# Kernel optimization log

Hardware: AMD Instinct MI355X
Metric: run time of the kernel (lower is better)

## Reference

```python
import jax, jax.numpy as jnp
import numpy as np

H = 512
N = 512
BSZ = 8
L = 4096
DIRECTION = 2  # 0=forward, 1=backward, 2=bidirectional (split N in half)


def setup_inputs() -> dict:
    key = jax.random.key(0)
    k = jax.random.split(key, 6)
    u = jax.random.normal(k[0], (BSZ, L, H), jnp.float32)
    # variable lengths in [L//2, L]
    lengths = jax.random.randint(k[1], (BSZ,), L // 2, L + 1).astype(jnp.int32)
    # LRU init: r_min=0, r_max=1, max_phase=2*pi
    u1 = jax.random.uniform(k[2], (N,), jnp.float32)
    nu_log = jnp.log(-0.5 * jnp.log(u1))
    u2 = jax.random.uniform(k[3], (N,), jnp.float32)
    theta_log = jnp.log(2.0 * np.pi * u2)
    lam = jnp.exp(-jnp.exp(nu_log) + 1j * jnp.exp(theta_log))  # (N,) complex
    gamma = jnp.sqrt(1.0 - jnp.abs(lam) ** 2)[:, None]          # (N,1)
    B = jax.random.normal(k[4], (H, N, 2), jnp.float32) / np.float32(np.sqrt(2 * H)) * gamma
    C = jax.random.normal(k[5], (2, H, N), jnp.float32) / np.float32(np.sqrt(N))
    return {"u": u, "lengths": lengths, "nu_log": nu_log, "theta_log": theta_log, "B": B, "C": C}


def _lru_scan(lam, Bu, reverse):
    """Diagonal linear recurrence x_t = lam * x_{t-1} + Bu_t along axis 2 via associative scan.
    lam: (n,) complex; Bu: (B, n, L) complex."""
    a = jnp.broadcast_to(lam[None, :, None], Bu.shape)

    def op(e1, e2):
        a1, b1 = e1
        a2, b2 = e2
        return a1 * a2, a2 * b1 + b2

    _, x = jax.lax.associative_scan(op, (a, Bu), axis=2, reverse=reverse)
    return x


def reference(u, lengths, nu_log, theta_log, B, C):
    lam = jnp.exp(-jnp.exp(nu_log) + 1j * jnp.exp(theta_log))  # (N,)
    Bc = B[..., 0] + 1j * B[..., 1]                            # (H, N) complex
    Bu = jnp.einsum('blh,hn->bnl', u, Bc)                      # (B, N, L) complex
    mask = jnp.arange(L)[None, :] < lengths[:, None]           # (B, L)
    Bu = Bu * mask[:, None, :]
    if DIRECTION == 2:
        h = N // 2
        x = jnp.concatenate([
            _lru_scan(lam[:h], Bu[:, :h], reverse=False),
            _lru_scan(lam[h:], Bu[:, h:], reverse=True),
        ], axis=1)
    elif DIRECTION == 0:
        x = _lru_scan(lam, Bu, reverse=False)
    else:
        x = _lru_scan(lam, Bu, reverse=True)
    x = x * mask[:, None, :]           # zero outputs past each sequence length
    x = jnp.swapaxes(x, 1, 2)          # (B, L, N)
    y = x.real @ C[0] - x.imag @ C[1]  # (B, L, H)  (requires H == N, as in source)
    return y
```

## Files before the change

kernel.cpp:

```cpp
#include <hip/hip_runtime.h>

#define L_SEQ   4096
#define BSZQ    8
#define ROWS    (BSZQ * L_SEQ)
#define KC1     512
#define NC1     1024
#define KC2     1024
#define NC2     512
#define CHUNK   64
#define NCHUNK  64

typedef __attribute__((ext_vector_type(8))) short bfrag;
typedef __attribute__((ext_vector_type(4))) float ffrag;

static __device__ __forceinline__ unsigned short f2bf(float f) {
    union { float f; unsigned int u; } v; v.f = f;
    unsigned int r = v.u + 0x7fffu + ((v.u >> 16) & 1u);
    return (unsigned short)(r >> 16);
}
static __device__ __forceinline__ unsigned int pk2(float a, float b) {
    return (unsigned int)f2bf(a) | ((unsigned int)f2bf(b) << 16);
}
static __device__ __forceinline__ float2 unpk2(unsigned int u) {
    union { unsigned int u; float f; } a, b;
    a.u = u << 16;
    b.u = u & 0xffff0000u;
    return make_float2(a.f, b.f);
}

static __device__ __forceinline__ void async16(const void* g, void* l) {
    __builtin_amdgcn_global_load_lds(
        (const __attribute__((address_space(1))) unsigned int*)g,
        (__attribute__((address_space(3))) unsigned int*)l,
        16, 0, 0);
}

__global__ __launch_bounds__(256) void prep_all_kernel(
    const float* __restrict__ B, const float* __restrict__ C,
    const float* __restrict__ nu_log, const float* __restrict__ theta_log,
    unsigned short* __restrict__ Bt, unsigned short* __restrict__ Dt,
    float2* __restrict__ lam)
{
    int g = blockIdx.x, tid = threadIdx.x;
    if (g < 2048) {
        int idx = g * 256 + tid;
        int n2 = idx >> 9, h = idx & 511;
        Bt[idx] = f2bf(B[(size_t)h * 1024 + n2]);
    } else if (g < 4096) {
        int idx = (g - 2048) * 256 + tid;
        int j = idx >> 10, k = idx & 1023;
        int n = k >> 1, c = k & 1;
        float v = C[((size_t)c * 512 + n) * 512 + j];
        Dt[idx] = f2bf(c ? -v : v);
    } else {
#pragma unroll
        for (int r = 0; r < 2; r++) {
            int n = tid + r * 256;
            float mag = expf(-expf(nu_log[n]));
            float th  = expf(theta_log[n]);
            lam[n] = make_float2(mag * cosf(th), mag * sinf(th));
        }
    }
}

__global__ __launch_bounds__(256) void conv_mask_kernel(
    const float* __restrict__ u, const int* __restrict__ lengths,
    unsigned short* __restrict__ ub)
{
    int idx = blockIdx.x * 256 + threadIdx.x;
    int row = idx >> 6;
    int l = row & (L_SEQ - 1), b = row >> 12;
    bool keep = (l < lengths[b]);
    union { unsigned int s[4]; float4 f; } o;
    if (keep) {
        const float4 a = *(const float4*)(u + (size_t)idx * 8);
        const float4 c = *(const float4*)(u + (size_t)idx * 8 + 4);
        o.s[0] = pk2(a.x, a.y); o.s[1] = pk2(a.z, a.w);
        o.s[2] = pk2(c.x, c.y); o.s[3] = pk2(c.z, c.w);
    } else {
        o.s[0] = o.s[1] = o.s[2] = o.s[3] = 0u;
    }
    *(float4*)(ub + (size_t)idx * 8) = o.f;
}

template<int KD, int ND, bool BF16OUT>
__global__ __launch_bounds__(256, 4) void gemm_db(
    const unsigned short* __restrict__ A,
    const unsigned short* __restrict__ Bt,
    void* __restrict__ Co)
{
    __shared__ __align__(16) unsigned short As[2][128 * 32];
    __shared__ __align__(16) unsigned short Bs[2][128 * 32];

    const int tid  = threadIdx.x;
    const int lane = tid & 63, w = tid >> 6;
    const int q = lane >> 4, m16 = lane & 15;
    const int wr = (w >> 1) * 64, wc = (w & 1) * 64;
    const int row0 = blockIdx.x * 128;
    const int col0 = blockIdx.y * 128;

    ffrag acc[4][4];
#pragma unroll
    for (int i = 0; i < 4; i++)
#pragma unroll
        for (int j = 0; j < 4; j++) acc[i][j] = (ffrag)0.f;

#define STAGE_T(GP, TB, KT, GR0) do {                                          \
    _Pragma("unroll")                                                          \
    for (int j_ = 0; j_ < 2; j_++) {                                           \
        int s_ = j_ * 256 + tid;                                               \
        int r_ = s_ >> 2;                                                      \
        int cs_ = (s_ & 3) ^ ((r_ >> 1) & 3);                                  \
        async16(GP + (size_t)((GR0) + r_) * KD + (KT) + cs_ * 8,               \
                &TB[(size_t)(j_ * 256 + w * 64) * 8]);                         \
    }                                                                          \
} while (0)

    STAGE_T(A,  As[0], 0, row0);
    STAGE_T(Bt, Bs[0], 0, col0);
    __syncthreads();

    int c = 0;
    for (int kt = 0; kt < KD; kt += 32) {
        if (kt + 32 < KD) {
            STAGE_T(A,  As[c ^ 1], kt + 32, row0);
            STAGE_T(Bt, Bs[c ^ 1], kt + 32, col0);
        }
        bfrag a[4], b[4];
#pragma unroll
        for (int ri = 0; ri < 4; ri++) {
            int r_ = wr + ri * 16 + m16;
            a[ri] = *(const bfrag*)&As[c][r_ * 32 + (q ^ ((r_ >> 1) & 3)) * 8];
        }
#pragma unroll
        for (int ci = 0; ci < 4; ci++) {
            int r_ = wc + ci * 16 + m16;
            b[ci] = *(const bfrag*)&Bs[c][r_ * 32 + (q ^ ((r_ >> 1) & 3)) * 8];
        }
#pragma unroll
        for (int ri = 0; ri < 4; ri++)
#pragma unroll
            for (int ci = 0; ci < 4; ci++)
                acc[ri][ci] = __builtin_amdgcn_mfma_f32_16x16x32_bf16(
                    a[ri], b[ci], acc[ri][ci], 0, 0, 0);
        __syncthreads();
        c ^= 1;
    }
#undef STAGE_T

    if (BF16OUT) {
        unsigned int* Cb = (unsigned int*)Co;
        const int colc0 = (col0 >> 1) + (w & 1) * 32;
#pragma unroll
        for (int ri = 0; ri < 4; ri++)
#pragma unroll
            for (int cp = 0; cp < 2; cp++)
#pragma unroll
                for (int r4 = 0; r4 < 4; r4++) {
                    float a0 = acc[ri][cp * 2][r4];
                    float a1 = acc[ri][cp * 2 + 1][r4];
                    float b0 = __shfl_xor(a0, 1);
                    float b1 = __shfl_xor(a1, 1);
                    unsigned int uo = (m16 & 1) ? pk2(b1, a1) : pk2(a0, b0);
                    int row = row0 + wr + ri * 16 + q * 4 + r4;
                    int ccol = (cp * 2 + (m16 & 1)) * 8 + (m16 >> 1);
                    Cb[(size_t)row * (ND / 2) + colc0 + ccol] = uo;
                }
    } else {
        float* Cf = (float*)Co;
#pragma unroll
        for (int ri = 0; ri < 4; ri++)
#pragma unroll
            for (int r4 = 0; r4 < 4; r4++) {
                int row = row0 + wr + ri * 16 + q * 4 + r4;
#pragma unroll
                for (int ci = 0; ci < 4; ci++) {
                    int col = col0 + wc + ci * 16 + m16;
                    Cf[(size_t)row * ND + col] = acc[ri][ci][r4];
                }
            }
    }
}

__global__ __launch_bounds__(256) void scan_states_kernel(
    const unsigned int* __restrict__ bu, const float2* __restrict__ lam,
    float2* __restrict__ states)
{
    int t = threadIdx.x;
    int b = blockIdx.x >> 6;
    int c = blockIdx.x & 63;
    float4 lm = *(const float4*)&lam[2 * t];
    float x0r = 0.f, x0i = 0.f, x1r = 0.f, x1i = 0.f;
    bool fwd = (t < 128);
    int l0 = fwd ? (c * CHUNK) : (c * CHUNK + CHUNK - 1);
    const unsigned int* p = bu + ((size_t)b * L_SEQ + l0) * 512 + 2 * t;
    ptrdiff_t step = fwd ? 512 : -512;
#pragma unroll 8
    for (int i = 0; i < CHUNK; i++) {
        uint2 v = *(const uint2*)p;
        float2 v0 = unpk2(v.x), v1 = unpk2(v.y);
        float n0r = lm.x * x0r - lm.y * x0i + v0.x;
        float n0i = lm.x * x0i + lm.y * x0r + v0.y;
        float n1r = lm.z * x1r - lm.w * x1i + v1.x;
        float n1i = lm.z * x1i + lm.w * x1r + v1.y;
        x0r = n0r; x0i = n0i; x1r = n1r; x1i = n1i;
        p += step;
    }
    *(float4*)&states[((size_t)b * NCHUNK + c) * 512 + 2 * t] =
        make_float4(x0r, x0i, x1r, x1i);
}

__global__ __launch_bounds__(256) void scan_fix_apply_kernel(
    unsigned int* __restrict__ bu, const float2* __restrict__ states,
    const float2* __restrict__ lam, const int* __restrict__ lengths)
{
    int t = threadIdx.x;
    int b = blockIdx.x >> 6;
    int c = blockIdx.x & 63;
    int len = lengths[b];
    bool fwd = (t < 128);
    float4 lm = *(const float4*)&lam[2 * t];

    float a0r = lm.x, a0i = lm.y, a1r = lm.z, a1i = lm.w;
#pragma unroll
    for (int i = 0; i < 6; i++) {
        float n0r = a0r * a0r - a0i * a0i; a0i = 2.f * a0r * a0i; a0r = n0r;
        float n1r = a1r * a1r - a1i * a1i; a1i = 2.f * a1r * a1i; a1r = n1r;
    }

    float c0r = 0.f, c0i = 0.f, c1r = 0.f, c1i = 0.f;
    for (int g = 0; g < 8; ++g) {
        float4 s[8];
#pragma unroll
        for (int k = 0; k < 8; ++k) {
            int cc = fwd ? (g * 8 + k) : (63 - (g * 8 + k));
            s[k] = *(const float4*)&states[((size_t)b * NCHUNK + cc) * 512 + 2 * t];
        }
#pragma unroll
        for (int k = 0; k < 8; ++k) {
            int cc = fwd ? (g * 8 + k) : (63 - (g * 8 + k));
            bool use = fwd ? (cc < c) : (cc > c);
            if (use) {
                float n0r = a0r * c0r - a0i * c0i + s[k].x;
                float n0i = a0r * c0i + a0i * c0r + s[k].y;
                float n1r = a1r * c1r - a1i * c1i + s[k].z;
                float n1i = a1r * c1i + a1i * c1r + s[k].w;
                c0r = n0r; c0i = n0i; c1r = n1r; c1i = n1i;
            }
        }
    }

    int l0 = fwd ? (c * CHUNK) : (c * CHUNK + CHUNK - 1);
    int dl = fwd ? 1 : -1;
    unsigned int* p = bu + ((size_t)b * L_SEQ + l0) * 512 + 2 * t;
    ptrdiff_t step = fwd ? 512 : -512;
    float x0r = c0r, x0i = c0i, x1r = c1r, x1i = c1i;
    int l = l0;
#pragma unroll 8
    for (int i = 0; i < CHUNK; i++) {
        uint2 v = *(const uint2*)p;
        float2 v0 = unpk2(v.x), v1 = unpk2(v.y);
        float n0r = lm.x * x0r - lm.y * x0i + v0.x;
        float n0i = lm.x * x0i + lm.y * x0r + v0.y;
        float n1r = lm.z * x1r - lm.w * x1i + v1.x;
        float n1i = lm.z * x1i + lm.w * x1r + v1.y;
        x0r = n0r; x0i = n0i; x1r = n1r; x1i = n1i;
        uint2 o2;
        o2.x = (l >= len) ? 0u : pk2(x0r, x0i);
        o2.y = (l >= len) ? 0u : pk2(x1r, x1i);
        *(uint2*)p = o2;
        p += step; l += dl;
    }
}

extern "C" void kernel_launch(void* const* d_in, const int* in_sizes, int n_in,
                              void* d_out, int out_size, void* d_ws, size_t ws_size,
                              hipStream_t stream)
{
    const float* u        = (const float*)d_in[0];
    const int*   lengths  = (const int*)  d_in[1];
    const float* nu_log   = (const float*)d_in[2];
    const float* theta_log= (const float*)d_in[3];
    const float* B        = (const float*)d_in[4];
    const float* C        = (const float*)d_in[5];
    float* y = (float*)d_out;

    char* wp = (char*)d_ws;
    float2* lam     = (float2*)wp;  wp += 4096;
    float2* states  = (float2*)wp;  wp += (size_t)BSZQ * NCHUNK * 512 * 8;
    unsigned int* bu = (unsigned int*)wp; wp += (size_t)ROWS * 512 * 4;
    unsigned short* ub = (unsigned short*)wp; wp += (size_t)ROWS * 512 * 2;
    unsigned short* Bt = (unsigned short*)wp; wp += (size_t)NC1 * KC1 * 2;
    unsigned short* Dt = (unsigned short*)wp; wp += (size_t)NC2 * KC2 * 2;

    prep_all_kernel<<<4097, 256, 0, stream>>>(B, C, nu_log, theta_log, Bt, Dt, lam);
    conv_mask_kernel<<<8192, 256, 0, stream>>>(u, lengths, ub);

    {
        dim3 grid(ROWS / 128, NC1 / 128);
        gemm_db<KC1, NC1, true><<<grid, 256, 0, stream>>>(ub, Bt, bu);
    }

    scan_states_kernel<<<BSZQ * NCHUNK, 256, 0, stream>>>(bu, lam, states);
    scan_fix_apply_kernel<<<BSZQ * NCHUNK, 256, 0, stream>>>(bu, states, lam, lengths);

    {
        dim3 grid(ROWS / 128, NC2 / 128);
        gemm_db<KC2, NC2, false><<<grid, 256, 0, stream>>>(
            (const unsigned short*)bu, Dt, y);
    }
}
```

Measured before the change: 273.6 us.

## Split chunk-carry combine into a separate kernel and merge prep with conversion

Before, each of the 64 chunk blocks of the fix/apply kernel rescanned all earlier chunk states to build its own carry. That is quadratic redundant work and heavy reads of the states buffer. Now a small combine kernel runs one sequential pass per batch and direction, writes a carries buffer, and the apply kernel just loads its carry. The prep and input-conversion kernels are also merged into one launch. The cost is an extra tiny, low-occupancy serial kernel launch (32 blocks of 64 threads) and an extra workspace buffer.

Result: faster. 263.1 us (-3.8%).

```diff
diff --git a/kernel.cpp b/kernel.cpp
--- a/kernel.cpp
+++ b/kernel.cpp
@@ -35,19 +35,35 @@
         16, 0, 0);
 }
 
-__global__ __launch_bounds__(256) void prep_all_kernel(
+__global__ __launch_bounds__(256) void prep_conv_kernel(
+    const float* __restrict__ u, const int* __restrict__ lengths,
     const float* __restrict__ B, const float* __restrict__ C,
     const float* __restrict__ nu_log, const float* __restrict__ theta_log,
-    unsigned short* __restrict__ Bt, unsigned short* __restrict__ Dt,
-    float2* __restrict__ lam)
+    unsigned short* __restrict__ ub, unsigned short* __restrict__ Bt,
+    unsigned short* __restrict__ Dt, float2* __restrict__ lam)
 {
     int g = blockIdx.x, tid = threadIdx.x;
-    if (g < 2048) {
+    if (g < 8192) {
         int idx = g * 256 + tid;
+        int row = idx >> 6;
+        int l = row & (L_SEQ - 1), b = row >> 12;
+        bool keep = (l < lengths[b]);
+        union { unsigned int s[4]; float4 f; } o;
+        if (keep) {
+            const float4 a = *(const float4*)(u + (size_t)idx * 8);
+            const float4 c = *(const float4*)(u + (size_t)idx * 8 + 4);
+            o.s[0] = pk2(a.x, a.y); o.s[1] = pk2(a.z, a.w);
+            o.s[2] = pk2(c.x, c.y); o.s[3] = pk2(c.z, c.w);
+        } else {
+            o.s[0] = o.s[1] = o.s[2] = o.s[3] = 0u;
+        }
+        *(float4*)(ub + (size_t)idx * 8) = o.f;
+    } else if (g < 10240) {
+        int idx = (g - 8192) * 256 + tid;
         int n2 = idx >> 9, h = idx & 511;
         Bt[idx] = f2bf(B[(size_t)h * 1024 + n2]);
-    } else if (g < 4096) {
-        int idx = (g - 2048) * 256 + tid;
+    } else if (g < 12288) {
+        int idx = (g - 10240) * 256 + tid;
         int j = idx >> 10, k = idx & 1023;
         int n = k >> 1, c = k & 1;
         float v = C[((size_t)c * 512 + n) * 512 + j];
@@ -61,26 +77,6 @@
             lam[n] = make_float2(mag * cosf(th), mag * sinf(th));
         }
     }
-}
-
-__global__ __launch_bounds__(256) void conv_mask_kernel(
-    const float* __restrict__ u, const int* __restrict__ lengths,
-    unsigned short* __restrict__ ub)
-{
-    int idx = blockIdx.x * 256 + threadIdx.x;
-    int row = idx >> 6;
-    int l = row & (L_SEQ - 1), b = row >> 12;
-    bool keep = (l < lengths[b]);
-    union { unsigned int s[4]; float4 f; } o;
-    if (keep) {
-        const float4 a = *(const float4*)(u + (size_t)idx * 8);
-        const float4 c = *(const float4*)(u + (size_t)idx * 8 + 4);
-        o.s[0] = pk2(a.x, a.y); o.s[1] = pk2(a.z, a.w);
-        o.s[2] = pk2(c.x, c.y); o.s[3] = pk2(c.z, c.w);
-    } else {
-        o.s[0] = o.s[1] = o.s[2] = o.s[3] = 0u;
-    }
-    *(float4*)(ub + (size_t)idx * 8) = o.f;
 }
 
 template<int KD, int ND, bool BF16OUT>
@@ -210,51 +206,62 @@
         make_float4(x0r, x0i, x1r, x1i);
 }
 
-__global__ __launch_bounds__(256) void scan_fix_apply_kernel(
-    unsigned int* __restrict__ bu, const float2* __restrict__ states,
+__global__ __launch_bounds__(64) void scan_combine_kernel(
+    const float2* __restrict__ states, float2* __restrict__ carries,
+    const float2* __restrict__ lam)
+{
+    int b = blockIdx.x >> 2;
+    int s = blockIdx.x & 3;
+    int np = s * 64 + threadIdx.x;
+    int n0 = 2 * np;
+    bool fwd = (s < 2);
+    float4 lm = *(const float4*)&lam[n0];
+
+    float a0r = lm.x, a0i = lm.y, a1r = lm.z, a1i = lm.w;
+#pragma unroll
+    for (int i = 0; i < 6; i++) {
+        float n0r_ = a0r * a0r - a0i * a0i; a0i = 2.f * a0r * a0i; a0r = n0r_;
+        float n1r_ = a1r * a1r - a1i * a1i; a1i = 2.f * a1r * a1i; a1r = n1r_;
+    }
+
+    float c0r = 0.f, c0i = 0.f, c1r = 0.f, c1i = 0.f;
+    for (int g = 0; g < 8; ++g) {
+        float4 st[8];
+#pragma unroll
+        for (int k = 0; k < 8; ++k) {
+            int cc = fwd ? (g * 8 + k) : (63 - (g * 8 + k));
+            st[k] = *(const float4*)&states[((size_t)b * NCHUNK + cc) * 512 + n0];
+        }
+#pragma unroll
+        for (int k = 0; k < 8; ++k) {
+            int cc = fwd ? (g * 8 + k) : (63 - (g * 8 + k));
+            *(float4*)&carries[((size_t)b * NCHUNK + cc) * 512 + n0] =
+                make_float4(c0r, c0i, c1r, c1i);
+            float n0r_ = a0r * c0r - a0i * c0i + st[k].x;
+            float n0i_ = a0r * c0i + a0i * c0r + st[k].y;
+            float n1r_ = a1r * c1r - a1i * c1i + st[k].z;
+            float n1i_ = a1r * c1i + a1i * c1r + st[k].w;
+            c0r = n0r_; c0i = n0i_; c1r = n1r_; c1i = n1i_;
+        }
+    }
+}
+
+__global__ __launch_bounds__(256) void scan_apply_kernel(
+    unsigned int* __restrict__ bu, const float2* __restrict__ carries,
     const float2* __restrict__ lam, const int* __restrict__ lengths)
 {
     int t = threadIdx.x;
     int b = blockIdx.x >> 6;
     int c = blockIdx.x & 63;
     int len = lengths[b];
+    float4 lm = *(const float4*)&lam[2 * t];
+    float4 cy = *(const float4*)&carries[((size_t)b * NCHUNK + c) * 512 + 2 * t];
     bool fwd = (t < 128);
-    float4 lm = *(const float4*)&lam[2 * t];
-
-    float a0r = lm.x, a0i = lm.y, a1r = lm.z, a1i = lm.w;
-#pragma unroll
-    for (int i = 0; i < 6; i++) {
-        float n0r = a0r * a0r - a0i * a0i; a0i = 2.f * a0r * a0i; a0r = n0r;
-        float n1r = a1r * a1r - a1i * a1i; a1i = 2.f * a1r * a1i; a1r = n1r;
-    }
-
-    float c0r = 0.f, c0i = 0.f, c1r = 0.f, c1i = 0.f;
-    for (int g = 0; g < 8; ++g) {
-        float4 s[8];
-#pragma unroll
-        for (int k = 0; k < 8; ++k) {
-            int cc = fwd ? (g * 8 + k) : (63 - (g * 8 + k));
-            s[k] = *(const float4*)&states[((size_t)b * NCHUNK + cc) * 512 + 2 * t];
-        }
-#pragma unroll
-        for (int k = 0; k < 8; ++k) {
-            int cc = fwd ? (g * 8 + k) : (63 - (g * 8 + k));
-            bool use = fwd ? (cc < c) : (cc > c);
-            if (use) {
-                float n0r = a0r * c0r - a0i * c0i + s[k].x;
-                float n0i = a0r * c0i + a0i * c0r + s[k].y;
-                float n1r = a1r * c1r - a1i * c1i + s[k].z;
-                float n1i = a1r * c1i + a1i * c1r + s[k].w;
-                c0r = n0r; c0i = n0i; c1r = n1r; c1i = n1i;
-            }
-        }
-    }
-
     int l0 = fwd ? (c * CHUNK) : (c * CHUNK + CHUNK - 1);
     int dl = fwd ? 1 : -1;
     unsigned int* p = bu + ((size_t)b * L_SEQ + l0) * 512 + 2 * t;
     ptrdiff_t step = fwd ? 512 : -512;
-    float x0r = c0r, x0i = c0i, x1r = c1r, x1i = c1i;
+    float x0r = cy.x, x0i = cy.y, x1r = cy.z, x1i = cy.w;
     int l = l0;
 #pragma unroll 8
     for (int i = 0; i < CHUNK; i++) {
@@ -288,13 +295,14 @@
     char* wp = (char*)d_ws;
     float2* lam     = (float2*)wp;  wp += 4096;
     float2* states  = (float2*)wp;  wp += (size_t)BSZQ * NCHUNK * 512 * 8;
+    float2* carries = (float2*)wp;  wp += (size_t)BSZQ * NCHUNK * 512 * 8;
     unsigned int* bu = (unsigned int*)wp; wp += (size_t)ROWS * 512 * 4;
     unsigned short* ub = (unsigned short*)wp; wp += (size_t)ROWS * 512 * 2;
     unsigned short* Bt = (unsigned short*)wp; wp += (size_t)NC1 * KC1 * 2;
     unsigned short* Dt = (unsigned short*)wp; wp += (size_t)NC2 * KC2 * 2;
 
-    prep_all_kernel<<<4097, 256, 0, stream>>>(B, C, nu_log, theta_log, Bt, Dt, lam);
-    conv_mask_kernel<<<8192, 256, 0, stream>>>(u, lengths, ub);
+    prep_conv_kernel<<<12289, 256, 0, stream>>>(
+        u, lengths, B, C, nu_log, theta_log, ub, Bt, Dt, lam);
 
     {
         dim3 grid(ROWS / 128, NC1 / 128);
@@ -302,7 +310,8 @@
     }
 
     scan_states_kernel<<<BSZQ * NCHUNK, 256, 0, stream>>>(bu, lam, states);
-    scan_fix_apply_kernel<<<BSZQ * NCHUNK, 256, 0, stream>>>(bu, states, lam, lengths);
+    scan_combine_kernel<<<BSZQ * 4, 64, 0, stream>>>(states, carries, lam);
+    scan_apply_kernel<<<BSZQ * NCHUNK, 256, 0, stream>>>(bu, carries, lam, lengths);
 
     {
         dim3 grid(ROWS / 128, NC2 / 128);
```
